# Kernel optimization log

Hardware: AMD Instinct MI355X
Metric: run time of the kernel (lower is better)

The kernel has to match this reference:

```python
import jax, jax.numpy as jnp
import numpy as np

B, C, L = 16, 256, 2048

def setup_inputs() -> dict:
    key = jax.random.key(0)
    k1, k2, k3, k4 = jax.random.split(key, 4)
    return {
        "proj_query": jax.random.normal(k1, (B, C, L), dtype=jnp.float32),
        "proj_key": jax.random.normal(k2, (B, C, L), dtype=jnp.float32),
        "proj_val": jax.random.normal(k3, (B, C, L), dtype=jnp.float32),
        "padding_mask": jax.random.uniform(k4, (B, 1, L), dtype=jnp.float32),
    }

def reference(proj_query, proj_key, proj_val, padding_mask):
    c = proj_query.shape[1]
    # energy[b,l,m] = sum_c Q[b,c,l] * K[b,c,m]  -> (B, L, L)
    energy = jnp.einsum("bcl,bcm->blm", proj_query, proj_key) / jnp.sqrt(jnp.float32(c))
    # log-additive padding mask (the tril mask in the source is dead code, never applied)
    logits = energy + jnp.log(padding_mask + 1e-9)
    attention = jax.nn.softmax(logits, axis=-1)
    # post-softmax multiplicative mask
    attention = attention * padding_mask
    # out[b,c,l] = sum_m V[b,c,m] * attention[b,l,m]  -> (B, C, L)
    out = jnp.einsum("bcm,blm->bcl", proj_val, attention)
    return out
```

## Files before the change

kernel.cpp:

```cpp
#include <hip/hip_runtime.h>
#include <hip/hip_bf16.h>

#define B_ 16
#define C_ 256
#define L_ 2048
#define MT 32

typedef __attribute__((ext_vector_type(8))) short bf16x8;
typedef __attribute__((ext_vector_type(4))) float f32x4;

#define CEXP 0.09016844005556021f

__device__ __forceinline__ short f2bf_rne(float f) {
    union { float f; unsigned u; } x; x.f = f;
    unsigned r = x.u + 0x7fffu + ((x.u >> 16) & 1u);
    return (short)(r >> 16);
}

__device__ __forceinline__ void gld_lds16(const void* g, void* l) {
    __builtin_amdgcn_global_load_lds(
        (const __attribute__((address_space(1))) void*)g,
        (__attribute__((address_space(3))) void*)l, 16, 0, 0);
}

__device__ __forceinline__ void barrier_lds_only() {
    asm volatile("" ::: "memory");
    __builtin_amdgcn_s_waitcnt(0xC07F);
    __builtin_amdgcn_s_barrier();
    asm volatile("" ::: "memory");
}

__global__ __launch_bounds__(256) void prepass_kernel(
        const float* __restrict__ Qin, const float* __restrict__ Kin,
        const float* __restrict__ Vin, const float* __restrict__ mask,
        short* __restrict__ Qt, short* __restrict__ Kt, short* __restrict__ Vb) {
    const int bid = blockIdx.x;
    const int t = threadIdx.x;
    if (bid < 1024) {
        __shared__ unsigned short tile[64 * 256];
        const int tens = bid >> 9;
        const int b  = (bid >> 5) & 15;
        const int l0 = (bid & 31) * 64;
        const float* __restrict__ src = tens ? Kin : Qin;
        short* __restrict__ dst = tens ? Kt : Qt;
        const float scale = tens ? 1.0f : CEXP;
        #pragma unroll
        for (int iter = 0; iter < 16; ++iter) {
            int idx = iter * 256 + t;
            int ci = idx >> 4;
            int lc = (idx & 15) * 4;
            float4 v = *(const float4*)(src + ((size_t)(b * C_ + ci)) * L_ + l0 + lc);
            float vv[4] = {v.x, v.y, v.z, v.w};
            #pragma unroll
            for (int j = 0; j < 4; ++j) {
                int l = lc + j;
                tile[l * 256 + (((ci >> 3) ^ (l & 31)) << 3) + (ci & 7)] =
                    (unsigned short)f2bf_rne(vv[j] * scale);
            }
        }
        __syncthreads();
        #pragma unroll
        for (int iter = 0; iter < 8; ++iter) {
            int li = iter * 8 + (t >> 5);
            int ck = t & 31;
            uint4 val = *(const uint4*)(tile + li * 256 + ((ck ^ (li & 31)) << 3));
            *(uint4*)(dst + ((size_t)(b * L_ + l0 + li)) * C_ + ck * 8) = val;
        }
    } else {
        size_t e = ((size_t)(bid - 1024) * 256 + t) * 8;
        int b = (int)(e >> 19);
        int m = (int)(e & (L_ - 1));
        const float4 v0 = *(const float4*)(Vin + e);
        const float4 v1 = *(const float4*)(Vin + e + 4);
        const float* mp = mask + ((size_t)b << 11) + m;
        const float4 m0 = *(const float4*)mp;
        const float4 m1 = *(const float4*)(mp + 4);
        uint4 o;
        o.x = (unsigned)(unsigned short)f2bf_rne(v0.x * m0.x)
            | ((unsigned)(unsigned short)f2bf_rne(v0.y * m0.y) << 16);
        o.y = (unsigned)(unsigned short)f2bf_rne(v0.z * m0.z)
            | ((unsigned)(unsigned short)f2bf_rne(v0.w * m0.w) << 16);
        o.z = (unsigned)(unsigned short)f2bf_rne(v1.x * m1.x)
            | ((unsigned)(unsigned short)f2bf_rne(v1.y * m1.y) << 16);
        o.w = (unsigned)(unsigned short)f2bf_rne(v1.z * m1.z)
            | ((unsigned)(unsigned short)f2bf_rne(v1.w * m1.w) << 16);
        *(uint4*)(Vb + e) = o;
    }
}

__device__ __forceinline__ void stage_tiles(const short* __restrict__ Ksrc,
                                            const short* __restrict__ Vsrc,
                                            short* Ks, short* Vs, int m0, int t) {
    #pragma unroll
    for (int rr = 0; rr < 4; ++rr) {
        int G = rr * 256 + t;
        int m = G >> 5, p = G & 31;
        gld_lds16(Ksrc + ((size_t)(m0 + m) << 8) + (p ^ m) * 8, Ks + G * 8);
    }
    #pragma unroll
    for (int rr = 0; rr < 4; ++rr) {
        int G = rr * 256 + t;
        int c = G >> 2, p = G & 3;
        int kc = (p ^ (c >> 1)) & 3;
        gld_lds16(Vsrc + (size_t)c * L_ + m0 + kc * 8, Vs + G * 8);
    }
}

__global__ __launch_bounds__(256, 2) void attn_main(
        const short* __restrict__ Qt,
        const short* __restrict__ Kt,
        const short* __restrict__ Vb,
        const float* __restrict__ mask,
        float* __restrict__ out) {
    __shared__ __align__(16) char smem[71168];
    short* KsB0 = (short*)smem;
    short* KsB1 = (short*)(smem + 16384);
    short* VsB0 = (short*)(smem + 32768);
    short* VsB1 = (short*)(smem + 49152);
    short* Pl   = (short*)(smem + 65536);
    float* Dsh  = (float*)(smem + 70656);

    const int t = threadIdx.x;
    const int w = t >> 6, lane = t & 63, q = lane >> 4, n = lane & 15;
    const int g = w & 1, mt = w >> 1;

    const int b  = blockIdx.x & 15;
    const int l0 = (blockIdx.x >> 4) * 64;

    bf16x8 qf[2][8];
    {
        const short* qbase = Qt + ((size_t)b * L_ + (l0 + 32 * g)) * C_;
        #pragma unroll
        for (int lt = 0; lt < 2; ++lt)
            #pragma unroll
            for (int ks = 0; ks < 8; ++ks)
                qf[lt][ks] = *(const bf16x8*)(qbase + (size_t)(16 * lt + n) * C_ + 32 * ks + 8 * q);
    }

    const f32x4 fzero = {0.f, 0.f, 0.f, 0.f};
    f32x4 Oacc[4][4];
    #pragma unroll
    for (int i = 0; i < 4; ++i)
        #pragma unroll
        for (int j = 0; j < 4; ++j) Oacc[i][j] = fzero;
    float dn[2][4] = {{0.f,0.f,0.f,0.f},{0.f,0.f,0.f,0.f}};

    const short* Ksrc = Kt + (size_t)b * (L_ * C_);
    const short* Vsrc = Vb + (size_t)b * (C_ * L_);
    const float* mrow = mask + (size_t)b * L_;

    stage_tiles(Ksrc, Vsrc, KsB0, VsB0, 0, t);
    float wv = mrow[16 * mt + n] + 1e-9f;

    for (int it = 0; it < L_ / MT; ++it) {
        const int cur = it & 1;
        const short* Ks = cur ? KsB1 : KsB0;
        const short* Vs = cur ? VsB1 : VsB0;

        __syncthreads();

        float nw = 0.f;
        if (it + 1 < L_ / MT) {
            stage_tiles(Ksrc, Vsrc, cur ? KsB0 : KsB1, cur ? VsB0 : VsB1, (it + 1) * MT, t);
            nw = mrow[(it + 1) * MT + 16 * mt + n] + 1e-9f;
        }

        const short* Krow = Ks + (16 * mt + n) * 256;
        f32x4 S0 = fzero, S1 = fzero;
        #pragma unroll
        for (int ks = 0; ks < 8; ++ks) {
            bf16x8 bf = *(const bf16x8*)(Krow + (((4 * ks + q) ^ (16 * mt + n)) << 3));
            S0 = __builtin_amdgcn_mfma_f32_16x16x32_bf16(qf[0][ks], bf, S0, 0, 0, 0);
            S1 = __builtin_amdgcn_mfma_f32_16x16x32_bf16(qf[1][ks], bf, S1, 0, 0, 0);
        }

        {
            short* Pb = Pl + (32 * g + 4 * q) * 40 + 16 * mt + n;
            #pragma unroll
            for (int r = 0; r < 4; ++r) {
                float p0 = wv * exp2f(S0[r]);
                dn[0][r] += p0;
                Pb[r * 40] = f2bf_rne(p0);
                float p1 = wv * exp2f(S1[r]);
                dn[1][r] += p1;
                Pb[(16 * 40) + r * 40] = f2bf_rne(p1);
            }
        }

        barrier_lds_only();

        bf16x8 af[4];
        #pragma unroll
        for (int lt = 0; lt < 4; ++lt)
            af[lt] = *(const bf16x8*)(Pl + (16 * lt + n) * 40 + q * 8);
        #pragma unroll
        for (int ct = 0; ct < 4; ++ct) {
            int c = 64 * w + 16 * ct + n;
            bf16x8 vf = *(const bf16x8*)(Vs + c * 32 + (((q ^ (c >> 1)) & 3) << 3));
            #pragma unroll
            for (int lt = 0; lt < 4; ++lt)
                Oacc[lt][ct] = __builtin_amdgcn_mfma_f32_16x16x32_bf16(af[lt], vf, Oacc[lt][ct], 0, 0, 0);
        }

        wv = nw;
    }

    __syncthreads();

    #pragma unroll
    for (int d = 1; d < 16; d <<= 1) {
        #pragma unroll
        for (int lt = 0; lt < 2; ++lt)
            #pragma unroll
            for (int r = 0; r < 4; ++r)
                dn[lt][r] += __shfl_xor(dn[lt][r], d, 64);
    }
    if (n == 0) {
        #pragma unroll
        for (int lt = 0; lt < 2; ++lt)
            #pragma unroll
            for (int r = 0; r < 4; ++r)
                Dsh[mt * 64 + 32 * g + 16 * lt + 4 * q + r] = dn[lt][r];
    }
    __syncthreads();

    float rden[4][4];
    #pragma unroll
    for (int lt = 0; lt < 4; ++lt)
        #pragma unroll
        for (int r = 0; r < 4; ++r) {
            int l = 16 * lt + 4 * q + r;
            rden[lt][r] = 1.0f / (Dsh[l] + Dsh[64 + l]);
        }

    float* Osh = (float*)smem;
    #pragma unroll
    for (int lt = 0; lt < 4; ++lt)
        #pragma unroll
        for (int ct = 0; ct < 4; ++ct) {
            int c = 64 * w + 16 * ct + n;
            #pragma unroll
            for (int r = 0; r < 4; ++r)
                Osh[c * 65 + 16 * lt + 4 * q + r] = Oacc[lt][ct][r] * rden[lt][r];
        }
    __syncthreads();
    float* orow = out + (size_t)b * (C_ * L_) + l0;
    #pragma unroll 8
    for (int i = 0; i < 64; ++i) {
        int c = 64 * w + i;
        orow[(size_t)c * L_ + lane] = Osh[c * 65 + lane];
    }
}

extern "C" void kernel_launch(void* const* d_in, const int* in_sizes, int n_in,
                              void* d_out, int out_size, void* d_ws, size_t ws_size,
                              hipStream_t stream) {
    const float* Q    = (const float*)d_in[0];
    const float* K    = (const float*)d_in[1];
    const float* V    = (const float*)d_in[2];
    const float* mask = (const float*)d_in[3];
    float* out = (float*)d_out;

    short* Qt = (short*)d_ws;
    short* Kt = Qt + (size_t)B_ * L_ * C_;
    short* Vb = Kt + (size_t)B_ * L_ * C_;

    prepass_kernel<<<5120, 256, 0, stream>>>(Q, K, V, mask, Qt, Kt, Vb);
    attn_main<<<512, 256, 0, stream>>>(Qt, Kt, Vb, mask, out);
}
```

Baseline: 231.6 us.

## Load Q directly in attention kernel, stream V to registers, drop LDS epilogue

The prepass no longer converts Q. The attention kernel reads fp32 Q, scales it and converts it to bf16 in registers, which saves one workspace write and read of Q. V fragments are now loaded straight from global memory into registers and double-buffered across a manually unrolled two-step loop, so the V LDS buffers go away and LDS use drops to about 38KB. The P-tile row mapping is permuted so each lane ends up with four consecutive rows, which lets the output be written directly as float4 stores without the LDS transpose. The trade-off is a strided scalar Q load per block and V global-load latency exposed in the main loop, plus higher register pressure.

```diff
diff --git a/kernel.cpp b/kernel.cpp
--- a/kernel.cpp
+++ b/kernel.cpp
@@ -31,31 +31,27 @@
 }
 
 __global__ __launch_bounds__(256) void prepass_kernel(
-        const float* __restrict__ Qin, const float* __restrict__ Kin,
-        const float* __restrict__ Vin, const float* __restrict__ mask,
-        short* __restrict__ Qt, short* __restrict__ Kt, short* __restrict__ Vb) {
+        const float* __restrict__ Kin, const float* __restrict__ Vin,
+        const float* __restrict__ mask,
+        short* __restrict__ Kt, short* __restrict__ Vb) {
     const int bid = blockIdx.x;
     const int t = threadIdx.x;
-    if (bid < 1024) {
+    if (bid < 512) {
         __shared__ unsigned short tile[64 * 256];
-        const int tens = bid >> 9;
-        const int b  = (bid >> 5) & 15;
+        const int b  = bid >> 5;
         const int l0 = (bid & 31) * 64;
-        const float* __restrict__ src = tens ? Kin : Qin;
-        short* __restrict__ dst = tens ? Kt : Qt;
-        const float scale = tens ? 1.0f : CEXP;
         #pragma unroll
         for (int iter = 0; iter < 16; ++iter) {
             int idx = iter * 256 + t;
             int ci = idx >> 4;
             int lc = (idx & 15) * 4;
-            float4 v = *(const float4*)(src + ((size_t)(b * C_ + ci)) * L_ + l0 + lc);
+            float4 v = *(const float4*)(Kin + ((size_t)(b * C_ + ci)) * L_ + l0 + lc);
             float vv[4] = {v.x, v.y, v.z, v.w};
             #pragma unroll
             for (int j = 0; j < 4; ++j) {
                 int l = lc + j;
                 tile[l * 256 + (((ci >> 3) ^ (l & 31)) << 3) + (ci & 7)] =
-                    (unsigned short)f2bf_rne(vv[j] * scale);
+                    (unsigned short)f2bf_rne(vv[j]);
             }
         }
         __syncthreads();
@@ -64,10 +60,10 @@
             int li = iter * 8 + (t >> 5);
             int ck = t & 31;
             uint4 val = *(const uint4*)(tile + li * 256 + ((ck ^ (li & 31)) << 3));
-            *(uint4*)(dst + ((size_t)(b * L_ + l0 + li)) * C_ + ck * 8) = val;
+            *(uint4*)(Kt + ((size_t)(b * L_ + l0 + li)) * C_ + ck * 8) = val;
         }
     } else {
-        size_t e = ((size_t)(bid - 1024) * 256 + t) * 8;
+        size_t e = ((size_t)(bid - 512) * 256 + t) * 8;
         int b = (int)(e >> 19);
         int m = (int)(e & (L_ - 1));
         const float4 v0 = *(const float4*)(Vin + e);
@@ -88,37 +84,71 @@
     }
 }
 
-__device__ __forceinline__ void stage_tiles(const short* __restrict__ Ksrc,
-                                            const short* __restrict__ Vsrc,
-                                            short* Ks, short* Vs, int m0, int t) {
+__device__ __forceinline__ void stage_K(const short* __restrict__ Ksrc,
+                                        short* Ks, int m0, int t) {
     #pragma unroll
     for (int rr = 0; rr < 4; ++rr) {
         int G = rr * 256 + t;
         int m = G >> 5, p = G & 31;
-        gld_lds16(Ksrc + ((size_t)(m0 + m) << 8) + (p ^ m) * 8, Ks + G * 8);
-    }
-    #pragma unroll
-    for (int rr = 0; rr < 4; ++rr) {
-        int G = rr * 256 + t;
-        int c = G >> 2, p = G & 3;
-        int kc = (p ^ (c >> 1)) & 3;
-        gld_lds16(Vsrc + (size_t)c * L_ + m0 + kc * 8, Vs + G * 8);
-    }
-}
+        gld_lds16(Ksrc + ((size_t)(m0 + m) << 8) + ((p ^ m) << 3), Ks + G * 8);
+    }
+}
+
+__device__ __forceinline__ void load_V(bf16x8 (&vf)[4], const short* __restrict__ Vw, int m0) {
+    #pragma unroll
+    for (int ct = 0; ct < 4; ++ct)
+        vf[ct] = *(const bf16x8*)(Vw + (size_t)(ct * 16) * L_ + m0);
+}
+
+#define ATTN_ITER(KS_CUR, KS_NXT, VF_CUR, VF_NXT, M0, GUARD)                               \
+  {                                                                                        \
+    __syncthreads();                   \
+    if (!(GUARD) || ((M0) + MT < L_)) {                                                    \
+      stage_K(Ksrc, KS_NXT, (M0) + MT, t);                                                 \
+      load_V(VF_NXT, Vw, (M0) + MT);                                                       \
+    }                                                                                      \
+    float wv = mrow[(M0) + 16 * mt + n] + 1e-9f;                                           \
+    f32x4 S0 = fzero, S1 = fzero;                                                          \
+    const short* Krow = KS_CUR + (16 * mt + n) * 256;                                      \
+    _Pragma("unroll")                                                                      \
+    for (int ks = 0; ks < 8; ++ks) {                                                       \
+      bf16x8 bf = *(const bf16x8*)(Krow + (((4 * ks + q) ^ (16 * mt + n)) << 3));          \
+      S0 = __builtin_amdgcn_mfma_f32_16x16x32_bf16(qf[0][ks], bf, S0, 0, 0, 0);            \
+      S1 = __builtin_amdgcn_mfma_f32_16x16x32_bf16(qf[1][ks], bf, S1, 0, 0, 0);            \
+    }                                                                                      \
+    _Pragma("unroll")                                                                      \
+    for (int r = 0; r < 4; ++r) {                                                          \
+      float p0 = wv * exp2f(S0[r]);                                                        \
+      dn[0][r] += p0;                                                                      \
+      Pw0[(4 * r) * 40] = f2bf_rne(p0);                                                    \
+      float p1 = wv * exp2f(S1[r]);                                                        \
+      dn[1][r] += p1;                                                                      \
+      Pw0[(16 + 4 * r) * 40] = f2bf_rne(p1);                                               \
+    }                                                                                      \
+    barrier_lds_only();                     \
+    bf16x8 af[4];                                                                          \
+    _Pragma("unroll")                                                                      \
+    for (int lt = 0; lt < 4; ++lt)                                                         \
+      af[lt] = *(const bf16x8*)(Pl + (16 * lt + 4 * (n & 3) + (n >> 2)) * 40 + 8 * q);     \
+    _Pragma("unroll")                                                                      \
+    for (int ct = 0; ct < 4; ++ct)                                                         \
+      _Pragma("unroll")                                                                    \
+      for (int lt = 0; lt < 4; ++lt)                                                       \
+        Oacc[lt][ct] =                                                                     \
+            __builtin_amdgcn_mfma_f32_16x16x32_bf16(af[lt], VF_CUR[ct], Oacc[lt][ct], 0, 0, 0); \
+  }
 
 __global__ __launch_bounds__(256, 2) void attn_main(
-        const short* __restrict__ Qt,
+        const float* __restrict__ Qin,
         const short* __restrict__ Kt,
         const short* __restrict__ Vb,
         const float* __restrict__ mask,
         float* __restrict__ out) {
-    __shared__ __align__(16) char smem[71168];
+    __shared__ __align__(16) char smem[38400];
     short* KsB0 = (short*)smem;
     short* KsB1 = (short*)(smem + 16384);
-    short* VsB0 = (short*)(smem + 32768);
-    short* VsB1 = (short*)(smem + 49152);
-    short* Pl   = (short*)(smem + 65536);
-    float* Dsh  = (float*)(smem + 70656);
+    short* Pl   = (short*)(smem + 32768);
+    float* Dsh  = (float*)(smem + 37888);
 
     const int t = threadIdx.x;
     const int w = t >> 6, lane = t & 63, q = lane >> 4, n = lane & 15;
@@ -127,85 +157,47 @@
     const int b  = blockIdx.x & 15;
     const int l0 = (blockIdx.x >> 4) * 64;
 
-    bf16x8 qf[2][8];
-    {
-        const short* qbase = Qt + ((size_t)b * L_ + (l0 + 32 * g)) * C_;
-        #pragma unroll
-        for (int lt = 0; lt < 2; ++lt)
-            #pragma unroll
-            for (int ks = 0; ks < 8; ++ks)
-                qf[lt][ks] = *(const bf16x8*)(qbase + (size_t)(16 * lt + n) * C_ + 32 * ks + 8 * q);
-    }
-
-    const f32x4 fzero = {0.f, 0.f, 0.f, 0.f};
-    f32x4 Oacc[4][4];
-    #pragma unroll
-    for (int i = 0; i < 4; ++i)
-        #pragma unroll
-        for (int j = 0; j < 4; ++j) Oacc[i][j] = fzero;
-    float dn[2][4] = {{0.f,0.f,0.f,0.f},{0.f,0.f,0.f,0.f}};
-
     const short* Ksrc = Kt + (size_t)b * (L_ * C_);
     const short* Vsrc = Vb + (size_t)b * (C_ * L_);
     const float* mrow = mask + (size_t)b * L_;
-
-    stage_tiles(Ksrc, Vsrc, KsB0, VsB0, 0, t);
-    float wv = mrow[16 * mt + n] + 1e-9f;
-
-    for (int it = 0; it < L_ / MT; ++it) {
-        const int cur = it & 1;
-        const short* Ks = cur ? KsB1 : KsB0;
-        const short* Vs = cur ? VsB1 : VsB0;
-
-        __syncthreads();
-
-        float nw = 0.f;
-        if (it + 1 < L_ / MT) {
-            stage_tiles(Ksrc, Vsrc, cur ? KsB0 : KsB1, cur ? VsB0 : VsB1, (it + 1) * MT, t);
-            nw = mrow[(it + 1) * MT + 16 * mt + n] + 1e-9f;
-        }
-
-        const short* Krow = Ks + (16 * mt + n) * 256;
-        f32x4 S0 = fzero, S1 = fzero;
-        #pragma unroll
-        for (int ks = 0; ks < 8; ++ks) {
-            bf16x8 bf = *(const bf16x8*)(Krow + (((4 * ks + q) ^ (16 * mt + n)) << 3));
-            S0 = __builtin_amdgcn_mfma_f32_16x16x32_bf16(qf[0][ks], bf, S0, 0, 0, 0);
-            S1 = __builtin_amdgcn_mfma_f32_16x16x32_bf16(qf[1][ks], bf, S1, 0, 0, 0);
-        }
-
-        {
-            short* Pb = Pl + (32 * g + 4 * q) * 40 + 16 * mt + n;
-            #pragma unroll
-            for (int r = 0; r < 4; ++r) {
-                float p0 = wv * exp2f(S0[r]);
-                dn[0][r] += p0;
-                Pb[r * 40] = f2bf_rne(p0);
-                float p1 = wv * exp2f(S1[r]);
-                dn[1][r] += p1;
-                Pb[(16 * 40) + r * 40] = f2bf_rne(p1);
+    const short* Vw   = Vsrc + (size_t)(64 * w + n) * L_ + 8 * q;
+    short* Pw0 = Pl + (32 * g + q) * 40 + 16 * mt + n;
+
+    bf16x8 qf[2][8];
+    {
+        const float* Qb = Qin + (size_t)b * (C_ * L_) + (l0 + 32 * g + n);
+        #pragma unroll
+        for (int lt = 0; lt < 2; ++lt)
+            #pragma unroll
+            for (int ks = 0; ks < 8; ++ks) {
+                bf16x8 v;
+                #pragma unroll
+                for (int j = 0; j < 8; ++j) {
+                    float f = Qb[(size_t)(32 * ks + 8 * q + j) * L_ + 16 * lt];
+                    v[j] = f2bf_rne(f * CEXP);
+                }
+                qf[lt][ks] = v;
             }
-        }
-
-        barrier_lds_only();
-
-        bf16x8 af[4];
-        #pragma unroll
-        for (int lt = 0; lt < 4; ++lt)
-            af[lt] = *(const bf16x8*)(Pl + (16 * lt + n) * 40 + q * 8);
-        #pragma unroll
-        for (int ct = 0; ct < 4; ++ct) {
-            int c = 64 * w + 16 * ct + n;
-            bf16x8 vf = *(const bf16x8*)(Vs + c * 32 + (((q ^ (c >> 1)) & 3) << 3));
-            #pragma unroll
-            for (int lt = 0; lt < 4; ++lt)
-                Oacc[lt][ct] = __builtin_amdgcn_mfma_f32_16x16x32_bf16(af[lt], vf, Oacc[lt][ct], 0, 0, 0);
-        }
-
-        wv = nw;
-    }
-
-    __syncthreads();
+    }
+
+    const f32x4 fzero = {0.f, 0.f, 0.f, 0.f};
+    f32x4 Oacc[4][4];
+    #pragma unroll
+    for (int i = 0; i < 4; ++i)
+        #pragma unroll
+        for (int j = 0; j < 4; ++j) Oacc[i][j] = fzero;
+    float dn[2][4] = {{0.f,0.f,0.f,0.f},{0.f,0.f,0.f,0.f}};
+
+    stage_K(Ksrc, KsB0, 0, t);
+    bf16x8 vfA[4], vfB[4];
+    load_V(vfA, Vw, 0);
+
+    #pragma unroll 1
+    for (int it2 = 0; it2 < L_ / MT / 2; ++it2) {
+        const int m0 = it2 * (2 * MT);
+        ATTN_ITER(KsB0, KsB1, vfA, vfB, m0, false)
+        ATTN_ITER(KsB1, KsB0, vfB, vfA, m0 + MT, true)
+    }
 
     #pragma unroll
     for (int d = 1; d < 16; d <<= 1) {
@@ -215,6 +207,7 @@
             for (int r = 0; r < 4; ++r)
                 dn[lt][r] += __shfl_xor(dn[lt][r], d, 64);
     }
+    __syncthreads();
     if (n == 0) {
         #pragma unroll
         for (int lt = 0; lt < 2; ++lt)
@@ -233,23 +226,19 @@
             rden[lt][r] = 1.0f / (Dsh[l] + Dsh[64 + l]);
         }
 
-    float* Osh = (float*)smem;
+    float* ob = out + (size_t)b * (C_ * L_) + l0;
     #pragma unroll
     for (int lt = 0; lt < 4; ++lt)
         #pragma unroll
         for (int ct = 0; ct < 4; ++ct) {
             int c = 64 * w + 16 * ct + n;
-            #pragma unroll
-            for (int r = 0; r < 4; ++r)
-                Osh[c * 65 + 16 * lt + 4 * q + r] = Oacc[lt][ct][r] * rden[lt][r];
-        }
-    __syncthreads();
-    float* orow = out + (size_t)b * (C_ * L_) + l0;
-    #pragma unroll 8
-    for (int i = 0; i < 64; ++i) {
-        int c = 64 * w + i;
-        orow[(size_t)c * L_ + lane] = Osh[c * 65 + lane];
-    }
+            float4 val;
+            val.x = Oacc[lt][ct][0] * rden[lt][0];
+            val.y = Oacc[lt][ct][1] * rden[lt][1];
+            val.z = Oacc[lt][ct][2] * rden[lt][2];
+            val.w = Oacc[lt][ct][3] * rden[lt][3];
+            *(float4*)(ob + (size_t)c * L_ + 16 * lt + 4 * q) = val;
+        }
 }
 
 extern "C" void kernel_launch(void* const* d_in, const int* in_sizes, int n_in,
@@ -261,10 +250,9 @@
     const float* mask = (const float*)d_in[3];
     float* out = (float*)d_out;
 
-    short* Qt = (short*)d_ws;
-    short* Kt = Qt + (size_t)B_ * L_ * C_;
+    short* Kt = (short*)d_ws;
     short* Vb = Kt + (size_t)B_ * L_ * C_;
 
-    prepass_kernel<<<5120, 256, 0, stream>>>(Q, K, V, mask, Qt, Kt, Vb);
-    attn_main<<<512, 256, 0, stream>>>(Qt, Kt, Vb, mask, out);
-}
+    prepass_kernel<<<4608, 256, 0, stream>>>(K, V, mask, Kt, Vb);
+    attn_main<<<512, 256, 0, stream>>>(Q, Kt, Vb, mask, out);
+}
```

Result: slower. 237.3 us (+2.5%).
